# Optimization experiments

Measured on AMD Instinct MI355X. Metric: run time of the kernel, lower is better.

The kernel has to match this reference:

```python
import jax, jax.numpy as jnp
import numpy as np


def setup_inputs() -> dict:
    key = jax.random.key(0)
    k1, k2, k3, k4 = jax.random.split(key, 4)
    B, C, H, W = 32, 2048, 24, 24
    MID = 256
    cam = jax.random.normal(k1, (B, C, H, W), dtype=jnp.float32)
    feat = jax.random.normal(k2, (B, C, H, W), dtype=jnp.float32)
    # 1x1 conv weights (no bias): [out_ch, in_ch]
    W1 = jax.random.normal(k3, (MID, C), dtype=jnp.float32) * (1.0 / np.sqrt(C))
    W2 = jax.random.normal(k4, (MID, C), dtype=jnp.float32) * (1.0 / np.sqrt(C))
    alpha = jnp.ones((), dtype=jnp.float32)
    return {"cam": cam, "feat": feat, "W1": W1, "W2": W2, "alpha": alpha}


def reference(cam, feat, W1, W2, alpha):
    B, C, H, W = cam.shape
    N = H * W
    feat_flat = feat.reshape(B, C, N)            # b c n
    f1 = jnp.einsum('mc,bcn->bmn', W1, feat_flat)  # 1x1 conv == channel GEMM
    f2 = jnp.einsum('mc,bcn->bmn', W2, feat_flat)
    attn = jnp.einsum('bmi,bmj->bij', f1, f2)    # b n n
    attn = jax.nn.softmax(attn, axis=-1)
    cam_flat = cam.reshape(B, C, N).transpose(0, 2, 1)  # b n c
    cam_refined = jnp.einsum('bij,bjc->bic', attn, cam_flat)  # b n c
    cam_refined = cam_refined.transpose(0, 2, 1).reshape(B, C, H, W)
    return alpha * cam_refined + cam
```

## Files before the change

### kernel.cpp

```cpp
#include <hip/hip_runtime.h>
#include <math.h>

typedef unsigned short u16;
typedef unsigned int u32;
typedef _Float16 f16;
typedef __attribute__((ext_vector_type(8))) _Float16 f16x8;
typedef __attribute__((ext_vector_type(4))) float f32x4;

static constexpr int B_   = 32;
static constexpr int C_   = 2048;
static constexpr int N_   = 576;
static constexpr int MID_ = 256;
static constexpr int M_   = 512;
static constexpr int NB_  = B_ * N_;

typedef const __attribute__((address_space(1))) unsigned int gu32_t;
typedef __attribute__((address_space(3))) unsigned int lu32_t;
__device__ __forceinline__ void gl16(const void* g, void* l) {
  __builtin_amdgcn_global_load_lds((gu32_t*)g, (lu32_t*)l, 16, 0, 0);
}

__global__ __launch_bounds__(256) void k_prep_w(
    const float* __restrict__ W1, const float* __restrict__ W2,
    f16* __restrict__ Wc) {
  const int e0 = (blockIdx.x * 256 + threadIdx.x) * 8;
  const int m = e0 >> 11;
  const int c = e0 & 2047;
  const float* src = (m < MID_) ? &W1[(size_t)m * C_ + c]
                                : &W2[(size_t)(m - MID_) * C_ + c];
  const float4 a = *(const float4*)&src[0];
  const float4 b = *(const float4*)&src[4];
  f16x8 hv;
  hv[0] = (f16)a.x; hv[1] = (f16)a.y; hv[2] = (f16)a.z; hv[3] = (f16)a.w;
  hv[4] = (f16)b.x; hv[5] = (f16)b.y; hv[6] = (f16)b.z; hv[7] = (f16)b.w;
  *(f16x8*)&Wc[e0] = hv;
}

__global__ __launch_bounds__(256) void k_prep_feat(
    const float* __restrict__ feat, f16* __restrict__ fT) {
  const int c0 = blockIdx.x * 64;
  const int n0 = blockIdx.y * 64;
  const int b  = blockIdx.z;
  __shared__ float Ts[64][65];
  const float* src = feat + ((size_t)b * C_ + c0) * N_ + n0;
  const int t = threadIdx.x;
  const int tr  = t >> 4;
  const int tc4 = (t & 15) * 4;
#pragma unroll
  for (int e = 0; e < 4; ++e) {
    const int c = tr + e * 16;
    const float4 v = *(const float4*)&src[(size_t)c * N_ + tc4];
    Ts[c][tc4] = v.x; Ts[c][tc4 + 1] = v.y;
    Ts[c][tc4 + 2] = v.z; Ts[c][tc4 + 3] = v.w;
  }
  __syncthreads();
  const int co = (t & 7) * 8;
#pragma unroll
  for (int p = 0; p < 2; ++p) {
    const int n = (t >> 3) + p * 32;
    f16x8 hv;
#pragma unroll
    for (int e = 0; e < 8; ++e) hv[e] = (f16)Ts[co + e][n];
    *(f16x8*)&fT[((size_t)b * N_ + n0 + n) * C_ + c0 + co] = hv;
  }
}

__global__ __launch_bounds__(256) void k_prep_cam(
    const float* __restrict__ cam, f16* __restrict__ camh) {
  const int e0 = (blockIdx.x * 256 + threadIdx.x) * 8;
  const float4 a = *(const float4*)&cam[e0];
  const float4 b = *(const float4*)&cam[e0 + 4];
  f16x8 hv;
  hv[0] = (f16)a.x; hv[1] = (f16)a.y; hv[2] = (f16)a.z; hv[3] = (f16)a.w;
  hv[4] = (f16)b.x; hv[5] = (f16)b.y; hv[6] = (f16)b.z; hv[7] = (f16)b.w;
  *(f16x8*)&camh[e0] = hv;
}

__global__ __launch_bounds__(256) void k_f12(
    const f16* __restrict__ fT, const f16* __restrict__ Wc,
    f16* __restrict__ f12) {
  const int mt = blockIdx.x;
  const int nt = blockIdx.y;
  __shared__ __align__(16) f16 As[128 * 32], Bs[128 * 32];
  const int t = threadIdx.x, lane = t & 63, w = t >> 6;
  const int wm = (w >> 1) * 64, wn = (w & 1) * 64;
  const int n0 = nt * 128, m0 = mt * 128;
  const int rrow = lane >> 2;
  const int koff = (lane & 3) * 8;
  const int r0 = w * 32;

  f32x4 acc[4][4];
#pragma unroll
  for (int i = 0; i < 4; ++i)
#pragma unroll
    for (int j = 0; j < 4; ++j) acc[i][j] = (f32x4)(0.0f);

  for (int k0 = 0; k0 < C_; k0 += 32) {
#pragma unroll
    for (int q = 0; q < 2; ++q) {
      const int row = r0 + q * 16 + rrow;
      const int lb = (r0 + q * 16) * 32;
      gl16(&fT[(size_t)(n0 + row) * C_ + k0 + koff], &As[lb]);
      gl16(&Wc[(size_t)(m0 + row) * C_ + k0 + koff], &Bs[lb]);
    }
    __syncthreads();
    const int fr = lane & 15, qo = (lane >> 4) * 8;
    f16x8 af[4], bf[4];
#pragma unroll
    for (int i = 0; i < 4; ++i) {
      af[i] = *(const f16x8*)&As[(wm + 16 * i + fr) * 32 + qo];
      bf[i] = *(const f16x8*)&Bs[(wn + 16 * i + fr) * 32 + qo];
    }
#pragma unroll
    for (int i = 0; i < 4; ++i)
#pragma unroll
      for (int j = 0; j < 4; ++j)
        acc[i][j] = __builtin_amdgcn_mfma_f32_16x16x32_f16(af[i], bf[j], acc[i][j], 0, 0, 0);
    __syncthreads();
  }
#pragma unroll
  for (int i = 0; i < 4; ++i) {
    const int nb = n0 + wm + 16 * i + ((lane >> 4) * 4);
#pragma unroll
    for (int j = 0; j < 4; ++j) {
      const int m = m0 + wn + 16 * j + (lane & 15);
#pragma unroll
      for (int r = 0; r < 4; ++r)
        f12[(size_t)(nb + r) * M_ + m] = (f16)acc[i][j][r];
    }
  }
}

__global__ __launch_bounds__(256) void k_logits(
    const f16* __restrict__ f12, float* __restrict__ logits) {
  const int jt = blockIdx.x;
  const int it = blockIdx.y;
  const int b  = blockIdx.z;
  __shared__ __align__(16) f16 As[128 * 32], Bs[128 * 32];
  const int t = threadIdx.x, lane = t & 63, w = t >> 6;
  const int wm = (w >> 1) * 64, wn = (w & 1) * 64;
  const int i0 = it * 128, j0 = jt * 128;
  const int rrow = lane >> 2;
  const int koff = (lane & 3) * 8;
  const int r0 = w * 32;
  const f16* f_b = f12 + (size_t)b * N_ * M_;

  f32x4 acc[4][4];
#pragma unroll
  for (int i = 0; i < 4; ++i)
#pragma unroll
    for (int j = 0; j < 4; ++j) acc[i][j] = (f32x4)(0.0f);

  for (int k0 = 0; k0 < MID_; k0 += 32) {
#pragma unroll
    for (int q = 0; q < 2; ++q) {
      const int row = r0 + q * 16 + rrow;
      const int ig = min(i0 + row, N_ - 1);
      const int jg = min(j0 + row, N_ - 1);
      const int lb = (r0 + q * 16) * 32;
      gl16(&f_b[(size_t)ig * M_ + k0 + koff], &As[lb]);
      gl16(&f_b[(size_t)jg * M_ + MID_ + k0 + koff], &Bs[lb]);
    }
    __syncthreads();
    const int fr = lane & 15, qo = (lane >> 4) * 8;
    f16x8 af[4], bf[4];
#pragma unroll
    for (int i = 0; i < 4; ++i) {
      af[i] = *(const f16x8*)&As[(wm + 16 * i + fr) * 32 + qo];
      bf[i] = *(const f16x8*)&Bs[(wn + 16 * i + fr) * 32 + qo];
    }
#pragma unroll
    for (int i = 0; i < 4; ++i)
#pragma unroll
      for (int j = 0; j < 4; ++j)
        acc[i][j] = __builtin_amdgcn_mfma_f32_16x16x32_f16(af[i], bf[j], acc[i][j], 0, 0, 0);
    __syncthreads();
  }
  float* log_b = logits + (size_t)b * N_ * N_;
#pragma unroll
  for (int i = 0; i < 4; ++i) {
    const int ibase = i0 + wm + 16 * i + ((lane >> 4) * 4);
#pragma unroll
    for (int j = 0; j < 4; ++j) {
      const int jj = j0 + wn + 16 * j + (lane & 15);
      if (jj < N_) {
#pragma unroll
        for (int r = 0; r < 4; ++r) {
          const int ii = ibase + r;
          if (ii < N_) log_b[(size_t)ii * N_ + jj] = acc[i][j][r];
        }
      }
    }
  }
}

__global__ __launch_bounds__(64) void k_softmax(
    const float* __restrict__ logits, f16* __restrict__ attn) {
  const int row = blockIdx.x;
  const float* p = logits + (size_t)row * N_;
  f16* o = attn + (size_t)row * N_;
  const int lane = threadIdx.x;
  float v[9];
  float mx = -INFINITY;
#pragma unroll
  for (int q = 0; q < 9; ++q) {
    v[q] = p[lane + q * 64];
    mx = fmaxf(mx, v[q]);
  }
#pragma unroll
  for (int off = 32; off > 0; off >>= 1) mx = fmaxf(mx, __shfl_down(mx, off));
  mx = __shfl(mx, 0);
  float s = 0.f;
#pragma unroll
  for (int q = 0; q < 9; ++q) {
    v[q] = __expf(v[q] - mx);
    s += v[q];
  }
#pragma unroll
  for (int off = 32; off > 0; off >>= 1) s += __shfl_down(s, off);
  s = __shfl(s, 0);
  const float inv = 1.0f / s;
#pragma unroll
  for (int q = 0; q < 9; ++q) o[lane + q * 64] = (f16)(v[q] * inv);
}

__global__ __launch_bounds__(256) void k_out(
    const f16* __restrict__ camh, const f16* __restrict__ attn,
    const float* __restrict__ alpha_p, float* __restrict__ out) {
  const int ct = blockIdx.x;
  const int it = blockIdx.y;
  const int b  = blockIdx.z;
  __shared__ __align__(16) f16 As[128 * 32], Bs[128 * 32];
  const int t = threadIdx.x, lane = t & 63, w = t >> 6;
  const int wm = (w >> 1) * 64, wn = (w & 1) * 64;
  const int c0 = ct * 128, i0 = it * 128;
  const int rrow = lane >> 2;
  const int koff = (lane & 3) * 8;
  const int r0 = w * 32;
  const f16* camh_b = camh + (size_t)b * C_ * N_;
  const f16* attn_b = attn + (size_t)b * N_ * N_;

  f32x4 acc[4][4];
#pragma unroll
  for (int i = 0; i < 4; ++i)
#pragma unroll
    for (int j = 0; j < 4; ++j) acc[i][j] = (f32x4)(0.0f);

  for (int k0 = 0; k0 < N_; k0 += 32) {
#pragma unroll
    for (int q = 0; q < 2; ++q) {
      const int row = r0 + q * 16 + rrow;
      const int cg = c0 + row;
      const int ig = min(i0 + row, N_ - 1);
      const int lb = (r0 + q * 16) * 32;
      gl16(&camh_b[(size_t)cg * N_ + k0 + koff], &As[lb]);
      gl16(&attn_b[(size_t)ig * N_ + k0 + koff], &Bs[lb]);
    }
    __syncthreads();
    const int fr = lane & 15, qo = (lane >> 4) * 8;
    f16x8 af[4], bf[4];
#pragma unroll
    for (int i = 0; i < 4; ++i) {
      af[i] = *(const f16x8*)&As[(wm + 16 * i + fr) * 32 + qo];
      bf[i] = *(const f16x8*)&Bs[(wn + 16 * i + fr) * 32 + qo];
    }
#pragma unroll
    for (int i = 0; i < 4; ++i)
#pragma unroll
      for (int j = 0; j < 4; ++j)
        acc[i][j] = __builtin_amdgcn_mfma_f32_16x16x32_f16(af[i], bf[j], acc[i][j], 0, 0, 0);
    __syncthreads();
  }
  const float alpha = *alpha_p;
  float* out_b = out + (size_t)b * C_ * N_;
#pragma unroll
  for (int ii = 0; ii < 4; ++ii) {
    const int c = c0 + wm + 16 * ii + ((lane >> 4) * 4);
#pragma unroll
    for (int jj = 0; jj < 4; ++jj) {
      const int i = i0 + wn + 16 * jj + (lane & 15);
      if (i < N_) {
#pragma unroll
        for (int r = 0; r < 4; ++r) {
          const size_t off = (size_t)(c + r) * N_ + i;
          out_b[off] = alpha * acc[ii][jj][r] + (float)camh_b[off];
        }
      }
    }
  }
}

extern "C" void kernel_launch(void* const* d_in, const int* in_sizes, int n_in,
                              void* d_out, int out_size, void* d_ws,
                              size_t ws_size, hipStream_t stream) {
  const float* cam   = (const float*)d_in[0];
  const float* feat  = (const float*)d_in[1];
  const float* W1    = (const float*)d_in[2];
  const float* W2    = (const float*)d_in[3];
  const float* alpha = (const float*)d_in[4];
  float* out = (float*)d_out;

  char* ws = (char*)d_ws;
  f16*   fT     = (f16*)ws;
  f16*   f12    = (f16*)(ws + 75497472);
  f16*   Wc     = (f16*)(ws + 94371840);
  float* logits = (float*)ws;
  f16*   attn   = (f16*)(ws + 75497472);
  f16*   camh   = (f16*)ws;

  k_prep_w<<<dim3(512), 256, 0, stream>>>(W1, W2, Wc);
  k_prep_feat<<<dim3(32, 9, B_), 256, 0, stream>>>(feat, fT);
  k_f12<<<dim3(4, 144), 256, 0, stream>>>(fT, Wc, f12);
  k_logits<<<dim3(5, 5, B_), 256, 0, stream>>>(f12, logits);
  k_softmax<<<dim3(B_ * N_), 64, 0, stream>>>(logits, attn);
  k_prep_cam<<<dim3(18432), 256, 0, stream>>>(cam, camh);
  k_out<<<dim3(16, 5, B_), 256, 0, stream>>>(camh, attn, alpha, out);
}
```

Baseline: 531.2 us.

## Double-buffer LDS tiles, XOR-swizzle LDS layout, pack four softmax rows per block

Each of the three MFMA GEMM kernels now uses two LDS buffers. The next K-tile is issued via global_load_lds while the current tile feeds the MFMAs, which removes one barrier per iteration and aims to overlap loads with compute. The 16-byte chunk column is XOR-swizzled by row bits on both the store and read side to reduce LDS bank conflicts. Softmax now runs four rows per 256-thread block instead of one row per 64-thread block, which cuts block count. The risks are doubled LDS use, which can lower occupancy, and the question of whether global_load_lds completion is properly waited on before the barrier.

Measured after the change: 544.0 us. 2.4% more time.

```diff
diff --git a/kernel.cpp b/kernel.cpp
--- a/kernel.cpp
+++ b/kernel.cpp
@@ -19,6 +19,7 @@
 __device__ __forceinline__ void gl16(const void* g, void* l) {
   __builtin_amdgcn_global_load_lds((gu32_t*)g, (lu32_t*)l, 16, 0, 0);
 }
+
 
 __global__ __launch_bounds__(256) void k_prep_w(
     const float* __restrict__ W1, const float* __restrict__ W2,
@@ -81,13 +82,15 @@
     f16* __restrict__ f12) {
   const int mt = blockIdx.x;
   const int nt = blockIdx.y;
-  __shared__ __align__(16) f16 As[128 * 32], Bs[128 * 32];
+  __shared__ __align__(16) f16 As[2][128 * 32], Bs[2][128 * 32];
   const int t = threadIdx.x, lane = t & 63, w = t >> 6;
   const int wm = (w >> 1) * 64, wn = (w & 1) * 64;
   const int n0 = nt * 128, m0 = mt * 128;
   const int rrow = lane >> 2;
-  const int koff = (lane & 3) * 8;
+  const int koff = ((lane & 3) ^ ((lane >> 3) & 3)) * 8;
   const int r0 = w * 32;
+  const int fr = lane & 15;
+  const int qo = (((lane >> 4) ^ ((lane >> 1) & 3)) * 8);
 
   f32x4 acc[4][4];
 #pragma unroll
@@ -95,21 +98,27 @@
 #pragma unroll
     for (int j = 0; j < 4; ++j) acc[i][j] = (f32x4)(0.0f);
 
-  for (int k0 = 0; k0 < C_; k0 += 32) {
+  auto stage = [&](int k0, int buf) {
 #pragma unroll
     for (int q = 0; q < 2; ++q) {
       const int row = r0 + q * 16 + rrow;
       const int lb = (r0 + q * 16) * 32;
-      gl16(&fT[(size_t)(n0 + row) * C_ + k0 + koff], &As[lb]);
-      gl16(&Wc[(size_t)(m0 + row) * C_ + k0 + koff], &Bs[lb]);
-    }
-    __syncthreads();
-    const int fr = lane & 15, qo = (lane >> 4) * 8;
+      gl16(&fT[(size_t)(n0 + row) * C_ + k0 + koff], &As[buf][lb]);
+      gl16(&Wc[(size_t)(m0 + row) * C_ + k0 + koff], &Bs[buf][lb]);
+    }
+  };
+
+  stage(0, 0);
+  __syncthreads();
+  int cur = 0;
+  for (int k0 = 0; k0 < C_; k0 += 32) {
+    const int nxt = cur ^ 1;
+    if (k0 + 32 < C_) stage(k0 + 32, nxt);
     f16x8 af[4], bf[4];
 #pragma unroll
     for (int i = 0; i < 4; ++i) {
-      af[i] = *(const f16x8*)&As[(wm + 16 * i + fr) * 32 + qo];
-      bf[i] = *(const f16x8*)&Bs[(wn + 16 * i + fr) * 32 + qo];
+      af[i] = *(const f16x8*)&As[cur][(wm + 16 * i + fr) * 32 + qo];
+      bf[i] = *(const f16x8*)&Bs[cur][(wn + 16 * i + fr) * 32 + qo];
     }
 #pragma unroll
     for (int i = 0; i < 4; ++i)
@@ -117,6 +126,7 @@
       for (int j = 0; j < 4; ++j)
         acc[i][j] = __builtin_amdgcn_mfma_f32_16x16x32_f16(af[i], bf[j], acc[i][j], 0, 0, 0);
     __syncthreads();
+    cur = nxt;
   }
 #pragma unroll
   for (int i = 0; i < 4; ++i) {
@@ -136,13 +146,15 @@
   const int jt = blockIdx.x;
   const int it = blockIdx.y;
   const int b  = blockIdx.z;
-  __shared__ __align__(16) f16 As[128 * 32], Bs[128 * 32];
+  __shared__ __align__(16) f16 As[2][128 * 32], Bs[2][128 * 32];
   const int t = threadIdx.x, lane = t & 63, w = t >> 6;
   const int wm = (w >> 1) * 64, wn = (w & 1) * 64;
   const int i0 = it * 128, j0 = jt * 128;
   const int rrow = lane >> 2;
-  const int koff = (lane & 3) * 8;
+  const int koff = ((lane & 3) ^ ((lane >> 3) & 3)) * 8;
   const int r0 = w * 32;
+  const int fr = lane & 15;
+  const int qo = (((lane >> 4) ^ ((lane >> 1) & 3)) * 8);
   const f16* f_b = f12 + (size_t)b * N_ * M_;
 
   f32x4 acc[4][4];
@@ -151,23 +163,29 @@
 #pragma unroll
     for (int j = 0; j < 4; ++j) acc[i][j] = (f32x4)(0.0f);
 
-  for (int k0 = 0; k0 < MID_; k0 += 32) {
+  auto stage = [&](int k0, int buf) {
 #pragma unroll
     for (int q = 0; q < 2; ++q) {
       const int row = r0 + q * 16 + rrow;
       const int ig = min(i0 + row, N_ - 1);
       const int jg = min(j0 + row, N_ - 1);
       const int lb = (r0 + q * 16) * 32;
-      gl16(&f_b[(size_t)ig * M_ + k0 + koff], &As[lb]);
-      gl16(&f_b[(size_t)jg * M_ + MID_ + k0 + koff], &Bs[lb]);
-    }
-    __syncthreads();
-    const int fr = lane & 15, qo = (lane >> 4) * 8;
+      gl16(&f_b[(size_t)ig * M_ + k0 + koff], &As[buf][lb]);
+      gl16(&f_b[(size_t)jg * M_ + MID_ + k0 + koff], &Bs[buf][lb]);
+    }
+  };
+
+  stage(0, 0);
+  __syncthreads();
+  int cur = 0;
+  for (int k0 = 0; k0 < MID_; k0 += 32) {
+    const int nxt = cur ^ 1;
+    if (k0 + 32 < MID_) stage(k0 + 32, nxt);
     f16x8 af[4], bf[4];
 #pragma unroll
     for (int i = 0; i < 4; ++i) {
-      af[i] = *(const f16x8*)&As[(wm + 16 * i + fr) * 32 + qo];
-      bf[i] = *(const f16x8*)&Bs[(wn + 16 * i + fr) * 32 + qo];
+      af[i] = *(const f16x8*)&As[cur][(wm + 16 * i + fr) * 32 + qo];
+      bf[i] = *(const f16x8*)&Bs[cur][(wn + 16 * i + fr) * 32 + qo];
     }
 #pragma unroll
     for (int i = 0; i < 4; ++i)
@@ -175,6 +193,7 @@
       for (int j = 0; j < 4; ++j)
         acc[i][j] = __builtin_amdgcn_mfma_f32_16x16x32_f16(af[i], bf[j], acc[i][j], 0, 0, 0);
     __syncthreads();
+    cur = nxt;
   }
   float* log_b = logits + (size_t)b * N_ * N_;
 #pragma unroll
@@ -194,12 +213,12 @@
   }
 }
 
-__global__ __launch_bounds__(64) void k_softmax(
+__global__ __launch_bounds__(256) void k_softmax(
     const float* __restrict__ logits, f16* __restrict__ attn) {
-  const int row = blockIdx.x;
+  const int row = blockIdx.x * 4 + (threadIdx.x >> 6);
+  const int lane = threadIdx.x & 63;
   const float* p = logits + (size_t)row * N_;
   f16* o = attn + (size_t)row * N_;
-  const int lane = threadIdx.x;
   float v[9];
   float mx = -INFINITY;
 #pragma unroll
@@ -230,13 +249,15 @@
   const int ct = blockIdx.x;
   const int it = blockIdx.y;
   const int b  = blockIdx.z;
-  __shared__ __align__(16) f16 As[128 * 32], Bs[128 * 32];
+  __shared__ __align__(16) f16 As[2][128 * 32], Bs[2][128 * 32];
   const int t = threadIdx.x, lane = t & 63, w = t >> 6;
   const int wm = (w >> 1) * 64, wn = (w & 1) * 64;
   const int c0 = ct * 128, i0 = it * 128;
   const int rrow = lane >> 2;
-  const int koff = (lane & 3) * 8;
+  const int koff = ((lane & 3) ^ ((lane >> 3) & 3)) * 8;
   const int r0 = w * 32;
+  const int fr = lane & 15;
+  const int qo = (((lane >> 4) ^ ((lane >> 1) & 3)) * 8);
   const f16* camh_b = camh + (size_t)b * C_ * N_;
   const f16* attn_b = attn + (size_t)b * N_ * N_;
 
@@ -246,23 +267,29 @@
 #pragma unroll
     for (int j = 0; j < 4; ++j) acc[i][j] = (f32x4)(0.0f);
 
-  for (int k0 = 0; k0 < N_; k0 += 32) {
+  auto stage = [&](int k0, int buf) {
 #pragma unroll
     for (int q = 0; q < 2; ++q) {
       const int row = r0 + q * 16 + rrow;
       const int cg = c0 + row;
       const int ig = min(i0 + row, N_ - 1);
       const int lb = (r0 + q * 16) * 32;
-      gl16(&camh_b[(size_t)cg * N_ + k0 + koff], &As[lb]);
-      gl16(&attn_b[(size_t)ig * N_ + k0 + koff], &Bs[lb]);
-    }
-    __syncthreads();
-    const int fr = lane & 15, qo = (lane >> 4) * 8;
+      gl16(&camh_b[(size_t)cg * N_ + k0 + koff], &As[buf][lb]);
+      gl16(&attn_b[(size_t)ig * N_ + k0 + koff], &Bs[buf][lb]);
+    }
+  };
+
+  stage(0, 0);
+  __syncthreads();
+  int cur = 0;
+  for (int k0 = 0; k0 < N_; k0 += 32) {
+    const int nxt = cur ^ 1;
+    if (k0 + 32 < N_) stage(k0 + 32, nxt);
     f16x8 af[4], bf[4];
 #pragma unroll
     for (int i = 0; i < 4; ++i) {
-      af[i] = *(const f16x8*)&As[(wm + 16 * i + fr) * 32 + qo];
-      bf[i] = *(const f16x8*)&Bs[(wn + 16 * i + fr) * 32 + qo];
+      af[i] = *(const f16x8*)&As[cur][(wm + 16 * i + fr) * 32 + qo];
+      bf[i] = *(const f16x8*)&Bs[cur][(wn + 16 * i + fr) * 32 + qo];
     }
 #pragma unroll
     for (int i = 0; i < 4; ++i)
@@ -270,6 +297,7 @@
       for (int j = 0; j < 4; ++j)
         acc[i][j] = __builtin_amdgcn_mfma_f32_16x16x32_f16(af[i], bf[j], acc[i][j], 0, 0, 0);
     __syncthreads();
+    cur = nxt;
   }
   const float alpha = *alpha_p;
   float* out_b = out + (size_t)b * C_ * N_;
@@ -312,7 +340,7 @@
   k_prep_feat<<<dim3(32, 9, B_), 256, 0, stream>>>(feat, fT);
   k_f12<<<dim3(4, 144), 256, 0, stream>>>(fT, Wc, f12);
   k_logits<<<dim3(5, 5, B_), 256, 0, stream>>>(f12, logits);
-  k_softmax<<<dim3(B_ * N_), 64, 0, stream>>>(logits, attn);
+  k_softmax<<<dim3(NB_ / 4), 256, 0, stream>>>(logits, attn);
   k_prep_cam<<<dim3(18432), 256, 0, stream>>>(cam, camh);
   k_out<<<dim3(16, 5, B_), 256, 0, stream>>>(camh, attn, alpha, out);
 }
```
